# Performance work log

Hardware: AMD Instinct MI355X
Metric: run time of the kernel (lower is better)

Reference implementation:

```python
import jax, jax.numpy as jnp
import numpy as np

IMG = 512
SIZES = (16, 32, 64, 128, 256)
FEAT_HW = (128, 64, 32, 16, 8)
STRIDES = tuple(IMG // h for h in FEAT_HW)
RATIOS = np.array([0.5, 1.0, 2.0])
PRE_NMS = 1000        # pre_nms_top_n['testing']
POST_NMS = 300        # post_nms_top_n['testing']
NMS_THRESH = 0.7
MIN_SIZE = 1e-3
BBOX_XFORM_CLIP = float(np.log(1000.0 / 16.0))


def _base_anchors(size):
    h_r = np.sqrt(RATIOS)
    w_r = 1.0 / h_r
    ws = w_r * size
    hs = h_r * size
    return np.round(np.stack([-ws, -hs, ws, hs], axis=1) / 2.0)  # [3,4]


def _level_anchors(size, stride, hw):
    ba = _base_anchors(size)
    s = np.arange(hw, dtype=np.float32) * stride
    yy, xx = np.meshgrid(s, s, indexing='ij')  # y-major like torchvision
    shifts = np.stack([xx.ravel(), yy.ravel(), xx.ravel(), yy.ravel()], axis=1)
    return (shifts[:, None, :] + ba[None, :, :]).reshape(-1, 4).astype(np.float32)


ANCHORS = [jnp.asarray(_level_anchors(SIZES[i], STRIDES[i], FEAT_HW[i])) for i in range(5)]


def _conv(x, w, b, pad):
    y = jax.lax.conv_general_dilated(x, w, (1, 1), [(pad, pad), (pad, pad)],
                                     dimension_numbers=('NCHW', 'OIHW', 'NCHW'))
    return y + b[None, :, None, None]


def _decode(deltas, anchors):
    # deltas [N,K,4], anchors [K,4]; BoxCoder weights (1,1,1,1)
    w = anchors[:, 2] - anchors[:, 0]
    h = anchors[:, 3] - anchors[:, 1]
    cx = anchors[:, 0] + 0.5 * w
    cy = anchors[:, 1] + 0.5 * h
    dx, dy = deltas[..., 0], deltas[..., 1]
    dw = jnp.minimum(deltas[..., 2], BBOX_XFORM_CLIP)
    dh = jnp.minimum(deltas[..., 3], BBOX_XFORM_CLIP)
    pcx = dx * w + cx
    pcy = dy * h + cy
    pw = jnp.exp(dw) * w
    ph = jnp.exp(dh) * h
    return jnp.stack([pcx - 0.5 * pw, pcy - 0.5 * ph,
                      pcx + 0.5 * pw, pcy + 0.5 * ph], axis=-1)


def _nms_single(boxes_off, scores_masked, boxes_raw, scores_raw):
    # greedy NMS over fixed POST_NMS steps; suppressed/invalid score = -1
    def step(s, _):
        i = jnp.argmax(s)
        ok = s[i] > -0.5
        b = boxes_off[i]
        lt = jnp.maximum(b[:2], boxes_off[:, :2])
        rb = jnp.minimum(b[2:], boxes_off[:, 2:])
        wh = jnp.clip(rb - lt, 0.0)
        inter = wh[:, 0] * wh[:, 1]
        area_i = (b[2] - b[0]) * (b[3] - b[1])
        areas = (boxes_off[:, 2] - boxes_off[:, 0]) * (boxes_off[:, 3] - boxes_off[:, 1])
        iou = inter / jnp.maximum(area_i + areas - inter, 1e-9)
        s = jnp.where(ok & (iou > NMS_THRESH), -1.0, s)
        s = s.at[i].set(-1.0)
        return s, (i, ok)

    _, (idx, ok) = jax.lax.scan(step, scores_masked, None, length=POST_NMS)
    out_b = jnp.where(ok[:, None], boxes_raw[idx], 0.0)
    out_s = jnp.where(ok, scores_raw[idx], 0.0)
    return out_b, out_s


def _rpn_forward(feats, conv_w, conv_b, cls_w, cls_b, bbox_w, bbox_b):
    all_s, all_b, lvl_ids = [], [], []
    for lvl, f in enumerate(feats):
        t = jax.nn.relu(_conv(f, conv_w, conv_b, 1))
        obj = _conv(t, cls_w, cls_b, 0)      # [N,3,H,W]
        reg = _conv(t, bbox_w, bbox_b, 0)    # [N,12,H,W]
        N, _, H, W = obj.shape
        obj = obj.transpose(0, 2, 3, 1).reshape(N, -1)  # (H,W,A) order
        reg = reg.reshape(N, 3, 4, H, W).transpose(0, 3, 4, 1, 2).reshape(N, -1, 4)
        boxes = _decode(reg, ANCHORS[lvl])              # [N,HWA,4]
        k = min(PRE_NMS, obj.shape[1])
        top_s, top_i = jax.lax.top_k(obj, k)
        boxes = jnp.take_along_axis(boxes, top_i[:, :, None], axis=1)
        all_s.append(top_s)
        all_b.append(boxes)
        lvl_ids.append(jnp.full((k,), float(lvl), dtype=jnp.float32))
    scores = jnp.concatenate(all_s, axis=1)   # [N,K]
    boxes = jnp.concatenate(all_b, axis=1)    # [N,K,4]
    lvl = jnp.concatenate(lvl_ids)            # [K]
    # clip to image (512x512)
    boxes = jnp.stack([jnp.clip(boxes[..., 0], 0.0, IMG), jnp.clip(boxes[..., 1], 0.0, IMG),
                       jnp.clip(boxes[..., 2], 0.0, IMG), jnp.clip(boxes[..., 3], 0.0, IMG)], axis=-1)
    valid = ((boxes[..., 2] - boxes[..., 0]) >= MIN_SIZE) & ((boxes[..., 3] - boxes[..., 1]) >= MIN_SIZE)
    prob = jax.nn.sigmoid(scores)
    masked = jnp.where(valid, prob, -1.0)
    # batched_nms trick: offset boxes per level so cross-level IoU is 0
    off = lvl * (IMG + 1.0)
    boxes_off = boxes + off[None, :, None]
    return jax.vmap(_nms_single)(boxes_off, masked, boxes, prob)


def setup_inputs() -> dict:
    key = jax.random.key(0)
    ks = jax.random.split(key, 12)
    N, C = 4, 256
    inp = {'images': jax.random.normal(ks[0], (N, 3, IMG, IMG), jnp.float32)}
    for i, hw in enumerate(FEAT_HW):
        inp[f'f{i}'] = jax.random.normal(ks[1 + i], (N, C, hw, hw), jnp.float32)
    inp['conv_w'] = jax.random.normal(ks[6], (C, C, 3, 3), jnp.float32) * 0.01
    inp['conv_b'] = jnp.zeros((C,), jnp.float32)
    inp['cls_w'] = jax.random.normal(ks[7], (3, C, 1, 1), jnp.float32) * 0.01
    inp['cls_b'] = jnp.zeros((3,), jnp.float32)
    inp['bbox_w'] = jax.random.normal(ks[8], (12, C, 1, 1), jnp.float32) * 0.01
    inp['bbox_b'] = jnp.zeros((12,), jnp.float32)
    return inp


def reference(images, f0, f1, f2, f3, f4, conv_w, conv_b, cls_w, cls_b, bbox_w, bbox_b):
    # images only determine the (static) image size used for clipping
    del images
    return _rpn_forward((f0, f1, f2, f3, f4), conv_w, conv_b, cls_w, cls_b, bbox_w, bbox_b)
```

## Files before the change

kernel.cpp:

```cpp
#include <hip/hip_runtime.h>

#define FULL_PER_IMG 65472
#define SEL_PER_IMG  3960
#define BBOX_CLIP    4.135166556742356f

__device__ __forceinline__ unsigned int sortkey(float f){
  unsigned int u = __float_as_uint(f);
  return (u & 0x80000000u) ? ~u : (u | 0x80000000u);
}

__global__ __launch_bounds__(256) void repack_w(const float* __restrict__ src,
                                                float* __restrict__ dst){
  int idx = blockIdx.x*256 + threadIdx.x;
  if (idx >= 589824) return;
  int co = idx & 255;
  int kt = idx >> 8;
  int ci = kt / 9, tap = kt % 9;
  dst[idx] = src[co*2304 + ci*9 + tap];
}

#define CHBUF 1536
#define SMEMF 4160

template<int TX, int H, int NBX>
__device__ void conv_level(int lb,
    const float* __restrict__ f, int strd, float asize, int full_off, float lvl,
    const float* __restrict__ wp, const float* __restrict__ conv_b,
    const float* __restrict__ cls_w, const float* __restrict__ cls_b,
    const float* __restrict__ bbox_w, const float* __restrict__ bbox_b,
    float* __restrict__ A_score, float* __restrict__ A_masked, float* __restrict__ A_boxoff,
    float* smem, float (*s_out)[16])
{
  constexpr int W    = H;
  constexpr int NBY  = H/2;
  constexpr int P    = 2*TX;
  constexpr int ROWW = TX + 4;
  constexpr int CIST = 4*ROWW;
  constexpr int CHFL = 32*CIST;
  constexpr int NSTG = (CHFL + 255)/256;

  const int xb = lb % NBX;
  const int yb = (lb / NBX) % NBY;
  const int n  = lb / (NBX*NBY);
  const int x0 = xb * TX;
  const int y0 = yb * 2;
  const int co = threadIdx.x;
  const float* Fn = f + (size_t)n*256*H*W;
  float* lds_stage = smem;
  float* lds_t     = smem;

  float acc[2][TX];
  #pragma unroll
  for (int o=0;o<2;o++)
    #pragma unroll
    for (int p=0;p<TX;p++) acc[o][p] = conv_b[co];

  int soff[NSTG];
  #pragma unroll
  for (int k=0;k<NSTG;k++){
    const int e  = co + k*256;
    const int cl = e / CIST;
    const int rem = e - cl*CIST;
    const int r  = rem / ROWW;
    const int j  = rem - r*ROWW;
    const int yg = y0 - 1 + r, xg = x0 - 1 + j;
    soff[k] = (e < CHFL && yg>=0 && yg<H && xg>=0 && xg<W)
            ? (cl*H + yg)*W + xg : -1;
  }

#define STAGE(CB, BUF) do {                                                  \
    const float* Fb_ = Fn + (size_t)(CB)*H*W;                                \
    float st_[NSTG];                                                         \
    _Pragma("unroll")                                                        \
    for (int k=0;k<NSTG;k++)                                                 \
      st_[k] = (soff[k] >= 0) ? Fb_[soff[k]] : 0.f;                          \
    _Pragma("unroll")                                                        \
    for (int k=0;k<NSTG;k++){                                                \
      const int e = co + k*256;                                              \
      if (e < CHFL) (BUF)[e] = st_[k];                                       \
    }                                                                        \
  } while(0)

#define CIFMA(SB, CL, WV) do {                                               \
    const float* bp_ = (SB) + (CL)*CIST;                                     \
    _Pragma("unroll")                                                        \
    for (int r=0;r<4;r++){                                                   \
      float rw_[ROWW];                                                       \
      _Pragma("unroll")                                                      \
      for (int q=0;q<ROWW/4;q++){                                            \
        float4 v_ = *(const float4*)(bp_ + r*ROWW + 4*q);                    \
        rw_[4*q+0]=v_.x; rw_[4*q+1]=v_.y;                                    \
        rw_[4*q+2]=v_.z; rw_[4*q+3]=v_.w;                                    \
      }                                                                      \
      if (r <= 2){                                                           \
        _Pragma("unroll")                                                    \
        for (int kx=0;kx<3;kx++){                                            \
          const float w_ = WV[r*3+kx];                                       \
          _Pragma("unroll")                                                  \
          for (int p=0;p<TX;p++) acc[0][p] = fmaf(w_, rw_[p+kx], acc[0][p]); \
        }                                                                    \
      }                                                                      \
      if (r >= 1){                                                           \
        _Pragma("unroll")                                                    \
        for (int kx=0;kx<3;kx++){                                            \
          const float w_ = WV[(r-1)*3+kx];                                   \
          _Pragma("unroll")                                                  \
          for (int p=0;p<TX;p++) acc[1][p] = fmaf(w_, rw_[p+kx], acc[1][p]); \
        }                                                                    \
      }                                                                      \
    }                                                                        \
  } while(0)

  STAGE(0, lds_stage);
  __syncthreads();

  for (int ch=0; ch<8; ++ch){
    const float* sb = lds_stage + (ch&1)*CHBUF;
    for (int cl=0; cl<32; ++cl){
      const int ci = ch*32 + cl;
      float wv[9];
      const float* wrow = wp + (size_t)ci*2304 + co;
      #pragma unroll
      for (int t=0;t<9;t++) wv[t] = wrow[t*256];
      CIFMA(sb, cl, wv);
    }
    if (ch<7){
      STAGE((ch+1)*32, lds_stage + ((ch+1)&1)*CHBUF);
      __syncthreads();
    }
  }
#undef STAGE
#undef CIFMA

  __syncthreads();

  #pragma unroll
  for (int o=0;o<2;o++)
    #pragma unroll
    for (int p=0;p<TX;p++) lds_t[(o*TX+p)*260+co] = fmaxf(acc[o][p], 0.f);
  __syncthreads();

  {
    const int p = threadIdx.x % P;
    const int o = threadIdx.x / P;
    if (o < 15){
      const float* w1 = (o<3) ? (cls_w + o*256) : (bbox_w + (o-3)*256);
      float s = (o<3) ? cls_b[o] : bbox_b[o-3];
      const float4* wl = (const float4*)w1;
      const float4* tl = (const float4*)(lds_t + p*260);
      #pragma unroll 8
      for (int c=0;c<64;c++){
        float4 a = wl[c], b = tl[c];
        s += a.x*b.x + a.y*b.y + a.z*b.z + a.w*b.w;
      }
      s_out[o][p] = s;
    }
  }
  __syncthreads();

  if (threadIdx.x < 3*P){
    const int p = threadIdx.x / 3;
    const int a = threadIdx.x % 3;
    const int px = p % TX;
    const int yo = y0 + p / TX;
    float sraw = s_out[a][p];
    float dx = s_out[3+a*4+0][p];
    float dy = s_out[3+a*4+1][p];
    float dw = fminf(s_out[3+a*4+2][p], BBOX_CLIP);
    float dh = fminf(s_out[3+a*4+3][p], BBOX_CLIP);
    float ratio = (a==0)?0.5f:((a==1)?1.0f:2.0f);
    float hr = sqrtf(ratio);
    float wh2 = rintf(asize / hr * 0.5f);
    float hh2 = rintf(asize * hr * 0.5f);
    float w = 2.f*wh2, h = 2.f*hh2;
    float cx = (float)((x0+px)*strd);
    float cy = (float)(yo*strd);
    float pcx = dx*w + cx, pcy = dy*h + cy;
    float pw = expf(dw)*w, ph = expf(dh)*h;
    float x1 = pcx - 0.5f*pw, y1 = pcy - 0.5f*ph;
    float x2 = pcx + 0.5f*pw, y2 = pcy + 0.5f*ph;
    x1 = fminf(fmaxf(x1,0.f),512.f); y1 = fminf(fmaxf(y1,0.f),512.f);
    x2 = fminf(fmaxf(x2,0.f),512.f); y2 = fminf(fmaxf(y2,0.f),512.f);
    bool valid = ((x2-x1) >= 1e-3f) && ((y2-y1) >= 1e-3f);
    float prob = 1.f/(1.f+expf(-sraw));
    float masked = valid ? prob : -1.f;
    float off = lvl*513.f;
    size_t gi = (size_t)n*FULL_PER_IMG + full_off + ((yo*W + (x0+px))*3 + a);
    A_score[gi]  = sraw;
    A_masked[gi] = masked;
    float4 bo; bo.x=x1+off; bo.y=y1+off; bo.z=x2+off; bo.w=y2+off;
    *(float4*)(A_boxoff + gi*4) = bo;
  }
}

__global__ __launch_bounds__(256)
void conv_all(
    const float* __restrict__ f0, const float* __restrict__ f1,
    const float* __restrict__ f2, const float* __restrict__ f3,
    const float* __restrict__ f4,
    const float* __restrict__ wp, const float* __restrict__ conv_b,
    const float* __restrict__ cls_w, const float* __restrict__ cls_b,
    const float* __restrict__ bbox_w, const float* __restrict__ bbox_b,
    float* __restrict__ A_score, float* __restrict__ A_masked, float* __restrict__ A_boxoff)
{
  __shared__ float smem[SMEMF];
  __shared__ float s_out[15][16];
  const int b = blockIdx.x;
  if (b < 4096)
    conv_level< 8,128,16>(b,      f0,  4,  16.f,     0, 0.f, wp, conv_b, cls_w, cls_b, bbox_w, bbox_b, A_score, A_masked, A_boxoff, smem, s_out);
  else if (b < 5120)
    conv_level< 8, 64, 8>(b-4096, f1,  8,  32.f, 49152, 1.f, wp, conv_b, cls_w, cls_b, bbox_w, bbox_b, A_score, A_masked, A_boxoff, smem, s_out);
  else if (b < 5376)
    conv_level< 8, 32, 4>(b-5120, f2, 16,  64.f, 61440, 2.f, wp, conv_b, cls_w, cls_b, bbox_w, bbox_b, A_score, A_masked, A_boxoff, smem, s_out);
  else if (b < 5504)
    conv_level< 4, 16, 4>(b-5376, f3, 32, 128.f, 64512, 3.f, wp, conv_b, cls_w, cls_b, bbox_w, bbox_b, A_score, A_masked, A_boxoff, smem, s_out);
  else
    conv_level< 4,  8, 2>(b-5504, f4, 64, 256.f, 65280, 4.f, wp, conv_b, cls_w, cls_b, bbox_w, bbox_b, A_score, A_masked, A_boxoff, smem, s_out);
}

__global__ __launch_bounds__(1024) void select_kernel(
    const float* __restrict__ A_score, const float* __restrict__ A_masked,
    const float* __restrict__ A_boxoff,
    float* __restrict__ C_masked, float* __restrict__ C_boxoff)
{
  const int b = blockIdx.x;
  const int tid = threadIdx.x;
  if (b >= 12){
    const int n = b - 12;
    if (tid < 960){
      size_t gF = (size_t)n*FULL_PER_IMG + 64512 + tid;
      size_t gS = (size_t)n*SEL_PER_IMG  + 3000 + tid;
      C_masked[gS] = A_masked[gF];
      *(float4*)(C_boxoff + gS*4) = *(const float4*)(A_boxoff + gF*4);
    }
    return;
  }
  const int n = b / 3, lvl = b % 3;
  const int HWAs[3]  = {49152, 12288, 3072};
  const int FOFF[3]  = {0, 49152, 61440};
  const int HWA = HWAs[lvl];
  const size_t baseF = (size_t)n*FULL_PER_IMG + FOFF[lvl];
  const size_t baseS = (size_t)n*SEL_PER_IMG + lvl*1000;
  const int k = 1000;

  __shared__ unsigned int hist[256];
  __shared__ unsigned int sh_prefix, sh_krem, sh_c0, sh_c1, sh_above;
  if (tid==0){ sh_prefix=0u; sh_krem=(unsigned)k; }
  __syncthreads();

  for (int pass=3; pass>=0; pass--){
    if (tid < 256) hist[tid]=0u;
    __syncthreads();
    unsigned int pfx = sh_prefix;
    for (int i=tid;i<HWA;i+=1024){
      unsigned int u = sortkey(A_score[baseF+i]);
      if (pass==3 || (u >> ((pass+1)*8)) == pfx)
        atomicAdd(&hist[(u>>(pass*8)) & 255u], 1u);
    }
    __syncthreads();
    if (tid==0){
      unsigned int krem = sh_krem, accum = 0u; int chosen = 0;
      for (int bb=255; bb>=0; bb--){
        if (accum + hist[bb] >= krem){ chosen = bb; break; }
        accum += hist[bb];
      }
      sh_krem   = krem - accum;
      sh_prefix = (pfx<<8) | (unsigned)chosen;
    }
    __syncthreads();
  }
  const unsigned int T = sh_prefix;
  if (tid==0){ sh_c0=0u; sh_c1=0u; sh_above = (unsigned)k - sh_krem; }
  __syncthreads();
  const unsigned int nAbove = sh_above, need = sh_krem;

  for (int i=tid;i<HWA;i+=1024){
    unsigned int u = sortkey(A_score[baseF+i]);
    int pos = -1;
    if (u > T) pos = (int)atomicAdd(&sh_c0,1u);
    else if (u == T){
      unsigned int t = atomicAdd(&sh_c1,1u);
      if (t < need) pos = (int)(nAbove + t);
    }
    if (pos >= 0){
      C_masked[baseS+pos] = A_masked[baseF+i];
      *(float4*)(C_boxoff + (baseS+pos)*4) = *(const float4*)(A_boxoff + (baseF+i)*4);
    }
  }
}

__global__ __launch_bounds__(256) void nms_kernel(
    const float* __restrict__ C_masked, const float* __restrict__ C_boxoff,
    float* __restrict__ out_b, float* __restrict__ out_s)
{
  const int n = blockIdx.x, tid = threadIdx.x;
  float  s[16];
  float4 b[16];
  #pragma unroll
  for (int j=0;j<16;j++){
    int i = tid*16 + j;
    if (i < SEL_PER_IMG){
      s[j] = C_masked[(size_t)n*SEL_PER_IMG + i];
      b[j] = *(const float4*)(C_boxoff + ((size_t)n*SEL_PER_IMG + i)*4);
    } else { s[j] = -2.f; b[j] = make_float4(0.f,0.f,0.f,0.f); }
  }
  __shared__ float wslot[2][4][6];

  for (int step=0; step<300; step++){
    float v = -3.f; int bi = 1<<30;
    #pragma unroll
    for (int j=0;j<16;j++){
      if (s[j] > v){ v = s[j]; bi = tid*16 + j; }
    }
    #pragma unroll
    for (int m=32; m>=1; m>>=1){
      float ov = __shfl_xor(v, m); int oi = __shfl_xor(bi, m);
      if (ov > v || (ov == v && oi < bi)){ v = ov; bi = oi; }
    }
    float (*slot)[6] = wslot[step & 1];
    #pragma unroll
    for (int j=0;j<16;j++){
      if (tid*16 + j == bi){
        const int w = tid >> 6;
        slot[w][0] = v; slot[w][1] = __int_as_float(bi);
        slot[w][2] = b[j].x; slot[w][3] = b[j].y;
        slot[w][4] = b[j].z; slot[w][5] = b[j].w;
      }
    }
    __syncthreads();
    float bv = slot[0][0]; int bidx = __float_as_int(slot[0][1]);
    float b0 = slot[0][2], b1 = slot[0][3], b2 = slot[0][4], b3 = slot[0][5];
    #pragma unroll
    for (int q=1;q<4;q++){
      float qv = slot[q][0]; int qi = __float_as_int(slot[q][1]);
      bool take = (qv > bv) || (qv == bv && qi < bidx);
      if (take){
        bv = qv; bidx = qi;
        b0 = slot[q][2]; b1 = slot[q][3]; b2 = slot[q][4]; b3 = slot[q][5];
      }
    }
    if (bv <= -0.5f) break;
    float area_i = (b2-b0)*(b3-b1);
    #pragma unroll
    for (int j=0;j<16;j++){
      float xx1 = fmaxf(b0, b[j].x), yy1 = fmaxf(b1, b[j].y);
      float xx2 = fminf(b2, b[j].z), yy2 = fminf(b3, b[j].w);
      float iw = fmaxf(xx2-xx1, 0.f), ih = fmaxf(yy2-yy1, 0.f);
      float inter = iw*ih;
      float aj = (b[j].z-b[j].x)*(b[j].w-b[j].y);
      float iou = inter / fmaxf(area_i + aj - inter, 1e-9f);
      if (iou > 0.7f) s[j] = -1.f;
    }
    if (tid == 0){
      int lvl = (bidx<1000)?0:((bidx<2000)?1:((bidx<3000)?2:((bidx<3768)?3:4)));
      float off = (float)lvl * 513.f;
      size_t ob = ((size_t)n*300 + step)*4;
      out_b[ob+0]=b0-off; out_b[ob+1]=b1-off; out_b[ob+2]=b2-off; out_b[ob+3]=b3-off;
      out_s[(size_t)n*300 + step] = bv;
    }
  }
}

extern "C" void kernel_launch(void* const* d_in, const int* in_sizes, int n_in,
                              void* d_out, int out_size, void* d_ws, size_t ws_size,
                              hipStream_t stream) {
  (void)in_sizes; (void)n_in; (void)ws_size;
  const float* f0     = (const float*)d_in[1];
  const float* f1     = (const float*)d_in[2];
  const float* f2     = (const float*)d_in[3];
  const float* f3     = (const float*)d_in[4];
  const float* f4     = (const float*)d_in[5];
  const float* conv_w = (const float*)d_in[6];
  const float* conv_b = (const float*)d_in[7];
  const float* cls_w  = (const float*)d_in[8];
  const float* cls_b  = (const float*)d_in[9];
  const float* bbox_w = (const float*)d_in[10];
  const float* bbox_b = (const float*)d_in[11];

  float* ws       = (float*)d_ws;
  float* wp       = ws;
  float* A_score  = wp       + 589824;
  float* A_masked = A_score  + 261888;
  float* A_boxoff = A_masked + 261888;
  float* C_masked = A_boxoff + 1047552;
  float* C_boxoff = C_masked + 15840;

  float* out_b = (float*)d_out;
  float* out_s = out_b + 4800;

  hipMemsetAsync(d_out, 0, (size_t)out_size*sizeof(float), stream);

  repack_w<<<2304, 256, 0, stream>>>(conv_w, wp);

  conv_all<<<5536, 256, 0, stream>>>(f0, f1, f2, f3, f4,
      wp, conv_b, cls_w, cls_b, bbox_w, bbox_b, A_score, A_masked, A_boxoff);

  select_kernel<<<16, 1024, 0, stream>>>(A_score, A_masked, A_boxoff, C_masked, C_boxoff);
  nms_kernel<<<4, 256, 0, stream>>>(C_masked, C_boxoff, out_b, out_s);
}
```

Before: 2.193 ms.

## Replace iterative argmax NMS with bitonic sort and sequential accept-check NMS

The NMS kernel now bitonic-sorts the candidate scores with their indices in shared memory. A single wavefront then walks the sorted list, testing each candidate against the already-accepted boxes in parallel and accepting it if none suppress it. This removes 300 rounds of a block-wide argmax reduction with barriers, and the suppression pass over all 3960 boxes on every round. In exchange it adds a full 4096-element sort with many barriers and a serial scan whose length depends on the suppression rate. Each scan step does a dependent global load of the box.

```diff
diff --git a/kernel.cpp b/kernel.cpp
--- a/kernel.cpp
+++ b/kernel.cpp
@@ -294,69 +294,73 @@
     float* __restrict__ out_b, float* __restrict__ out_s)
 {
   const int n = blockIdx.x, tid = threadIdx.x;
-  float  s[16];
-  float4 b[16];
+  __shared__ unsigned long long keys[4096];
+  __shared__ float accb[304][4];
+
   #pragma unroll
-  for (int j=0;j<16;j++){
-    int i = tid*16 + j;
+  for (int s=0; s<16; ++s){
+    int i = s*256 + tid;
+    unsigned long long kk = 0ull;
     if (i < SEL_PER_IMG){
-      s[j] = C_masked[(size_t)n*SEL_PER_IMG + i];
-      b[j] = *(const float4*)(C_boxoff + ((size_t)n*SEL_PER_IMG + i)*4);
-    } else { s[j] = -2.f; b[j] = make_float4(0.f,0.f,0.f,0.f); }
-  }
-  __shared__ float wslot[2][4][6];
-
-  for (int step=0; step<300; step++){
-    float v = -3.f; int bi = 1<<30;
+      unsigned int sk = sortkey(C_masked[(size_t)n*SEL_PER_IMG + i]);
+      kk = ((unsigned long long)sk << 32) | (unsigned int)(~(unsigned int)i);
+    }
+    keys[i] = kk;
+  }
+  __syncthreads();
+
+  for (int k = 2; k <= 4096; k <<= 1){
+    for (int j = k >> 1; j > 0; j >>= 1){
+      #pragma unroll
+      for (int s=0; s<16; ++s){
+        int i = s*256 + tid;
+        int ixj = i ^ j;
+        if (ixj > i){
+          unsigned long long a = keys[i], b = keys[ixj];
+          bool up = ((i & k) == 0);
+          bool sw = up ? (a < b) : (a > b);
+          if (sw){ keys[i] = b; keys[ixj] = a; }
+        }
+      }
+      __syncthreads();
+    }
+  }
+
+  if (tid >= 64) return;
+  const unsigned int THRK = sortkey(-0.5f);
+  int nAcc = 0;
+  for (int i = 0; i < 4096 && nAcc < 300; ++i){
+    unsigned long long kk = keys[i];
+    unsigned int khi = (unsigned int)(kk >> 32);
+    if (khi <= THRK) break;
+    int idx = (int)(~(unsigned int)kk);
+    float4 bx = *(const float4*)(C_boxoff + ((size_t)n*SEL_PER_IMG + idx)*4);
+    bool sup = false;
     #pragma unroll
-    for (int j=0;j<16;j++){
-      if (s[j] > v){ v = s[j]; bi = tid*16 + j; }
-    }
-    #pragma unroll
-    for (int m=32; m>=1; m>>=1){
-      float ov = __shfl_xor(v, m); int oi = __shfl_xor(bi, m);
-      if (ov > v || (ov == v && oi < bi)){ v = ov; bi = oi; }
-    }
-    float (*slot)[6] = wslot[step & 1];
-    #pragma unroll
-    for (int j=0;j<16;j++){
-      if (tid*16 + j == bi){
-        const int w = tid >> 6;
-        slot[w][0] = v; slot[w][1] = __int_as_float(bi);
-        slot[w][2] = b[j].x; slot[w][3] = b[j].y;
-        slot[w][4] = b[j].z; slot[w][5] = b[j].w;
+    for (int q=0; q<5; ++q){
+      int a = tid + q*64;
+      if (a < nAcc){
+        float a0=accb[a][0], a1=accb[a][1], a2=accb[a][2], a3=accb[a][3];
+        float xx1 = fmaxf(a0, bx.x), yy1 = fmaxf(a1, bx.y);
+        float xx2 = fminf(a2, bx.z), yy2 = fminf(a3, bx.w);
+        float iw = fmaxf(xx2-xx1, 0.f), ih = fmaxf(yy2-yy1, 0.f);
+        float inter = iw*ih;
+        float ar_a = (a2-a0)*(a3-a1);
+        float ar_b = (bx.z-bx.x)*(bx.w-bx.y);
+        float iou = inter / fmaxf(ar_a + ar_b - inter, 1e-9f);
+        sup |= (iou > 0.7f);
       }
     }
-    __syncthreads();
-    float bv = slot[0][0]; int bidx = __float_as_int(slot[0][1]);
-    float b0 = slot[0][2], b1 = slot[0][3], b2 = slot[0][4], b3 = slot[0][5];
-    #pragma unroll
-    for (int q=1;q<4;q++){
-      float qv = slot[q][0]; int qi = __float_as_int(slot[q][1]);
-      bool take = (qv > bv) || (qv == bv && qi < bidx);
-      if (take){
-        bv = qv; bidx = qi;
-        b0 = slot[q][2]; b1 = slot[q][3]; b2 = slot[q][4]; b3 = slot[q][5];
+    if (__ballot(sup) == 0ull){
+      if (tid == 0){
+        accb[nAcc][0]=bx.x; accb[nAcc][1]=bx.y; accb[nAcc][2]=bx.z; accb[nAcc][3]=bx.w;
+        int lvl = (idx<1000)?0:((idx<2000)?1:((idx<3000)?2:((idx<3768)?3:4)));
+        float off = (float)lvl * 513.f;
+        size_t ob = ((size_t)n*300 + nAcc)*4;
+        out_b[ob+0]=bx.x-off; out_b[ob+1]=bx.y-off; out_b[ob+2]=bx.z-off; out_b[ob+3]=bx.w-off;
+        out_s[(size_t)n*300 + nAcc] = C_masked[(size_t)n*SEL_PER_IMG + idx];
       }
-    }
-    if (bv <= -0.5f) break;
-    float area_i = (b2-b0)*(b3-b1);
-    #pragma unroll
-    for (int j=0;j<16;j++){
-      float xx1 = fmaxf(b0, b[j].x), yy1 = fmaxf(b1, b[j].y);
-      float xx2 = fminf(b2, b[j].z), yy2 = fminf(b3, b[j].w);
-      float iw = fmaxf(xx2-xx1, 0.f), ih = fmaxf(yy2-yy1, 0.f);
-      float inter = iw*ih;
-      float aj = (b[j].z-b[j].x)*(b[j].w-b[j].y);
-      float iou = inter / fmaxf(area_i + aj - inter, 1e-9f);
-      if (iou > 0.7f) s[j] = -1.f;
-    }
-    if (tid == 0){
-      int lvl = (bidx<1000)?0:((bidx<2000)?1:((bidx<3000)?2:((bidx<3768)?3:4)));
-      float off = (float)lvl * 513.f;
-      size_t ob = ((size_t)n*300 + step)*4;
-      out_b[ob+0]=b0-off; out_b[ob+1]=b1-off; out_b[ob+2]=b2-off; out_b[ob+3]=b3-off;
-      out_s[(size_t)n*300 + step] = bv;
+      ++nAcc;
     }
   }
 }
```

Result: faster. 1.868 ms (-14.8%).
